# Kernel tuning notes

Measured on AMD Instinct MI355X. Metric: run time of the kernel, lower is better.

## Reference

```python
import jax, jax.numpy as jnp
import numpy as np
from jax import lax

B, T, D_IN, D_PROJ, D_OUT, LORDER = 16, 2048, 1024, 512, 1024, 20


def setup_inputs() -> dict:
    key = jax.random.key(0)
    k1, k2, k3, k4 = jax.random.split(key, 4)
    s = 0.05
    return {
        "input": jax.random.normal(k1, (B, T, D_IN), dtype=jnp.float32),
        "in_cache": jnp.zeros((B, D_PROJ, LORDER - 1), dtype=jnp.float32),
        "W_lin": jax.random.normal(k2, (D_IN, D_PROJ), dtype=jnp.float32) * s,
        "conv_w": jax.random.normal(k3, (D_PROJ, LORDER), dtype=jnp.float32) * s,
        "W_aff": jax.random.normal(k4, (D_PROJ, D_OUT), dtype=jnp.float32) * s,
        "b_aff": jnp.zeros((D_OUT,), dtype=jnp.float32),
    }


def reference(input, in_cache, W_lin, conv_w, W_aff, b_aff):
    L = conv_w.shape[1]
    # 1) linear down-projection (no bias): [B,T,Din] -> [B,T,Dp]
    x = jnp.einsum("btd,dp->btp", input, W_lin)
    # 2) FSMN causal depthwise memory block with streaming cache
    xt = jnp.swapaxes(x, 1, 2)                       # [B,Dp,T]
    cat = jnp.concatenate([in_cache, xt], axis=2)    # [B,Dp,T+L-1]
    out_cache = cat[:, :, -(L - 1):]                 # last L-1 frames for next chunk
    # depthwise conv over time, VALID padding -> output length T
    y = lax.conv_general_dilated(
        cat, conv_w[:, None, :],                      # rhs [Dp,1,L]
        window_strides=(1,), padding="VALID",
        dimension_numbers=("NCH", "OIH", "NCH"),
        feature_group_count=conv_w.shape[0])
    m = jnp.swapaxes(y + xt, 1, 2)                   # residual add, back to [B,T,Dp]
    # 3) affine up-projection + 4) ReLU
    out = jax.nn.relu(jnp.einsum("btp,po->bto", m, W_aff) + b_aff)
    return (out, out_cache)
```

## Files before the change

kernel.cpp:

```cpp
#include <hip/hip_runtime.h>
#include <cstdint>
#include <cstddef>

#define B_  16
#define T_  2048
#define DIN 1024
#define DPJ 512
#define DOUT 1024
#define LORD 20
#define HALO (LORD - 1)
#define M_ROWS (B_ * T_)
#define OUT0_ELEMS ((size_t)M_ROWS * DOUT)
#define CACHE_ELEMS ((size_t)B_ * DPJ * (LORD - 1))

typedef __bf16 bf16_t;
typedef __bf16 bf16x2 __attribute__((ext_vector_type(2)));
typedef __bf16 bf16x4 __attribute__((ext_vector_type(4)));
typedef __bf16 bf16x8 __attribute__((ext_vector_type(8)));
typedef float  f32x4  __attribute__((ext_vector_type(4)));

__device__ __forceinline__ void async_load16(const void* g, void* lds_base) {
    __builtin_amdgcn_global_load_lds(
        (const __attribute__((address_space(1))) unsigned int*)g,
        (__attribute__((address_space(3))) unsigned int*)lds_base,
        16, 0, 0);
}

__device__ __forceinline__ int xcd_swizzle(int hw, int nwg) {
    int cpx = nwg >> 3;
    return (hw & 7) * cpx + (hw >> 3);
}

__global__ __launch_bounds__(256) void prep_weights(
    const float* __restrict__ Wl, const float* __restrict__ Wa,
    bf16_t* __restrict__ WlT, bf16_t* __restrict__ WaT) {
    int idx = blockIdx.x * 256 + threadIdx.x;
    const int n1 = DIN * DPJ;
    if (idx < n1) {
        int n = idx >> 10;
        int k = idx - (n << 10);
        WlT[idx] = (bf16_t)Wl[(size_t)k * DPJ + n];
    } else {
        int j = idx - n1;
        if (j < DPJ * DOUT) {
            int n = j >> 9;
            int k = j - (n << 9);
            WaT[j] = (bf16_t)Wa[(size_t)k * DOUT + n];
        }
    }
}

__global__ __launch_bounds__(512, 4) void gemm1_fused(
    const float* __restrict__ A, const bf16_t* __restrict__ Bt,
    bf16_t* __restrict__ C, const int M, const int N, const int K) {
    __shared__ bf16_t sA[2][128 * 64];
    __shared__ bf16_t sB[2][128 * 64];

    const int tid  = threadIdx.x;
    const int lane = tid & 63;
    const int wave = tid >> 6;

    const int gx   = gridDim.x;
    const int hw   = blockIdx.y * gx + blockIdx.x;
    const int lid  = xcd_swizzle(hw, gx * gridDim.y);
    const int lby  = lid / gx;
    const int lbx  = lid - lby * gx;
    const int col0 = lbx * 128;
    const int row0 = lby * 128;

    const int s4   = tid & 3;
    const int arow = tid >> 2;
    const float* gA = A + (size_t)(row0 + arow) * K + s4 * 8;
    const int o0 = ((s4       ^ (arow & 7)) << 3);
    const int o1 = (((s4 + 4) ^ (arow & 7)) << 3);

    const int lr  = lane >> 3;
    const int jsw = (lane & 7) ^ lr;
    const bf16_t* gB0 = Bt + (size_t)(col0 + wave * 16 + lr) * K + jsw * 8;

    const int wm = (wave >> 2) * 64;
    const int wn = (wave & 3) * 32;
    const int fr = lane & 15;
    const int fk = lane >> 4;

    const f32x4 zero = {0.f, 0.f, 0.f, 0.f};
    f32x4 acc[4][2];
#pragma unroll
    for (int mt = 0; mt < 4; ++mt)
#pragma unroll
        for (int nt = 0; nt < 2; ++nt) acc[mt][nt] = zero;

    f32x4 P[4], Q[4];

    auto load_a = [&](f32x4* r, int kk) {
        r[0] = *(const f32x4*)(gA + kk);
        r[1] = *(const f32x4*)(gA + kk + 4);
        r[2] = *(const f32x4*)(gA + kk + 32);
        r[3] = *(const f32x4*)(gA + kk + 36);
    };
    auto cvt_write = [&](const f32x4* r, bf16_t* dstbuf) {
        bf16x8 v0 = { (bf16_t)r[0][0], (bf16_t)r[0][1], (bf16_t)r[0][2], (bf16_t)r[0][3],
                      (bf16_t)r[1][0], (bf16_t)r[1][1], (bf16_t)r[1][2], (bf16_t)r[1][3] };
        bf16x8 v1 = { (bf16_t)r[2][0], (bf16_t)r[2][1], (bf16_t)r[2][2], (bf16_t)r[2][3],
                      (bf16_t)r[3][0], (bf16_t)r[3][1], (bf16_t)r[3][2], (bf16_t)r[3][3] };
        *(bf16x8*)(dstbuf + arow * 64 + o0) = v0;
        *(bf16x8*)(dstbuf + arow * 64 + o1) = v1;
    };
    auto stage_b = [&](int kk, bf16_t* dstbuf) {
#pragma unroll
        for (int c = 0; c < 2; ++c)
            async_load16(gB0 + (size_t)c * 8 * K + kk, dstbuf + wave * 1024 + c * 512);
    };
    auto compute = [&](const bf16_t* bA, const bf16_t* bB) {
#pragma unroll
        for (int h = 0; h < 2; ++h) {
            bf16x8 af[4], bfr[2];
#pragma unroll
            for (int mt = 0; mt < 4; ++mt) {
                int r = wm + mt * 16 + fr;
                int j = h * 4 + fk;
                af[mt] = *(const bf16x8*)(bA + r * 64 + ((j ^ (r & 7)) << 3));
            }
#pragma unroll
            for (int nt = 0; nt < 2; ++nt) {
                int r = wn + nt * 16 + fr;
                int j = h * 4 + fk;
                bfr[nt] = *(const bf16x8*)(bB + r * 64 + ((j ^ (r & 7)) << 3));
            }
#pragma unroll
            for (int mt = 0; mt < 4; ++mt)
#pragma unroll
                for (int nt = 0; nt < 2; ++nt)
                    acc[mt][nt] = __builtin_amdgcn_mfma_f32_16x16x32_bf16(
                        af[mt], bfr[nt], acc[mt][nt], 0, 0, 0);
        }
    };

    load_a(P, 0);
    stage_b(0, sB[0]);
    cvt_write(P, sA[0]);
    load_a(P, 64);

    for (int k0 = 0; k0 < K; k0 += 128) {
        asm volatile("s_waitcnt vmcnt(4) lgkmcnt(0)" ::: "memory");
        __builtin_amdgcn_sched_barrier(0);
        __builtin_amdgcn_s_barrier();
        __builtin_amdgcn_sched_barrier(0);
        {
            const int kn = k0 + 64;
            stage_b(kn, sB[1]);
            cvt_write(P, sA[1]);
            if (kn + 64 < K) load_a(Q, kn + 64);
        }
        compute(sA[0], sB[0]);

        const int kn2 = k0 + 128;
        if (kn2 >= K) {
            asm volatile("s_waitcnt vmcnt(0) lgkmcnt(0)" ::: "memory");
        } else {
            asm volatile("s_waitcnt vmcnt(4) lgkmcnt(0)" ::: "memory");
        }
        __builtin_amdgcn_sched_barrier(0);
        __builtin_amdgcn_s_barrier();
        __builtin_amdgcn_sched_barrier(0);
        if (kn2 < K) {
            stage_b(kn2, sB[0]);
            cvt_write(Q, sA[0]);
            if (kn2 + 64 < K) load_a(P, kn2 + 64);
        }
        compute(sA[1], sB[1]);
    }

    const int er = row0 + wm + (lane >> 4) * 4;
    const int ec = col0 + wn + (lane & 15);
#pragma unroll
    for (int mt = 0; mt < 4; ++mt)
#pragma unroll
        for (int nt = 0; nt < 2; ++nt)
#pragma unroll
            for (int rr = 0; rr < 4; ++rr)
                C[(size_t)(er + mt * 16 + rr) * N + (ec + nt * 16)] =
                    (bf16_t)acc[mt][nt][rr];
}

__global__ __launch_bounds__(256) void gemm_bt_relu(
    const bf16_t* __restrict__ A, const bf16_t* __restrict__ Bt,
    float* __restrict__ C, const float* __restrict__ bias,
    const int M, const int N, const int K) {
    __shared__ bf16_t sA[2][128 * 64];
    __shared__ bf16_t sB[2][128 * 64];

    const int tid  = threadIdx.x;
    const int lane = tid & 63;
    const int wave = tid >> 6;

    const int gx   = gridDim.x;
    const int hw   = blockIdx.y * gx + blockIdx.x;
    const int lid  = xcd_swizzle(hw, gx * gridDim.y);
    const int lby  = lid / gx;
    const int lbx  = lid - lby * gx;
    const int col0 = lbx * 128;
    const int row0 = lby * 128;

    const int lr   = lane >> 3;
    const int jsw  = (lane & 7) ^ lr;
    const bf16_t* gA0 = A  + (size_t)(row0 + wave * 32 + lr) * K + jsw * 8;
    const bf16_t* gB0 = Bt + (size_t)(col0 + wave * 32 + lr) * K + jsw * 8;

    const int wm = (wave >> 1) * 64;
    const int wn = (wave & 1) * 64;
    const int fr = lane & 15;
    const int fk = lane >> 4;

    const f32x4 zero = {0.f, 0.f, 0.f, 0.f};
    f32x4 acc[4][4];
#pragma unroll
    for (int mt = 0; mt < 4; ++mt)
#pragma unroll
        for (int nt = 0; nt < 4; ++nt) acc[mt][nt] = zero;

    auto stage = [&](int kk, bf16_t* dA, bf16_t* dB) {
#pragma unroll
        for (int c = 0; c < 4; ++c) {
            async_load16(gA0 + (size_t)c * 8 * K + kk, dA + wave * 2048 + c * 512);
            async_load16(gB0 + (size_t)c * 8 * K + kk, dB + wave * 2048 + c * 512);
        }
    };
    auto compute = [&](const bf16_t* bA, const bf16_t* bB) {
#pragma unroll
        for (int h = 0; h < 2; ++h) {
            bf16x8 af[4], bfr[4];
#pragma unroll
            for (int mt = 0; mt < 4; ++mt) {
                int r = wm + mt * 16 + fr;
                int j = h * 4 + fk;
                af[mt] = *(const bf16x8*)(bA + r * 64 + ((j ^ (r & 7)) << 3));
            }
#pragma unroll
            for (int nt = 0; nt < 4; ++nt) {
                int r = wn + nt * 16 + fr;
                int j = h * 4 + fk;
                bfr[nt] = *(const bf16x8*)(bB + r * 64 + ((j ^ (r & 7)) << 3));
            }
#pragma unroll
            for (int mt = 0; mt < 4; ++mt)
#pragma unroll
                for (int nt = 0; nt < 4; ++nt)
                    acc[mt][nt] = __builtin_amdgcn_mfma_f32_16x16x32_bf16(
                        af[mt], bfr[nt], acc[mt][nt], 0, 0, 0);
        }
    };

    stage(0, sA[0], sB[0]);

    for (int k0 = 0; k0 < K; k0 += 128) {
        asm volatile("s_waitcnt vmcnt(0)" ::: "memory");
        __builtin_amdgcn_sched_barrier(0);
        __builtin_amdgcn_s_barrier();
        __builtin_amdgcn_sched_barrier(0);
        stage(k0 + 64, sA[1], sB[1]);
        compute(sA[0], sB[0]);

        asm volatile("s_waitcnt vmcnt(0)" ::: "memory");
        __builtin_amdgcn_sched_barrier(0);
        __builtin_amdgcn_s_barrier();
        __builtin_amdgcn_sched_barrier(0);
        const int kn2 = k0 + 128;
        if (kn2 < K) stage(kn2, sA[0], sB[0]);
        compute(sA[1], sB[1]);
    }

    const int er = row0 + wm + (lane >> 4) * 4;
    const int ec = col0 + wn + (lane & 15);
#pragma unroll
    for (int nt = 0; nt < 4; ++nt) {
        float bb = bias[ec + nt * 16];
#pragma unroll
        for (int mt = 0; mt < 4; ++mt)
#pragma unroll
            for (int rr = 0; rr < 4; ++rr) {
                float v = acc[mt][nt][rr] + bb;
                C[(size_t)(er + mt * 16 + rr) * N + (ec + nt * 16)] =
                    v > 0.f ? v : 0.f;
            }
    }
}

#define TT 64
#define PPT 128
__global__ __launch_bounds__(256) void dwconv_tiled(
    const bf16_t* __restrict__ x, const float* __restrict__ cache,
    const float* __restrict__ cw, bf16_t* __restrict__ m,
    float* __restrict__ oc) {
    __shared__ float sx[(TT + HALO) * PPT];

    const int tid = threadIdx.x;
    const int t0  = blockIdx.x * TT;
    const int b   = blockIdx.y;
    const int p0  = blockIdx.z * PPT;

    for (int c = tid; c < (TT + HALO) * PPT / 8; c += 256) {
        int r    = c >> 4;
        int col  = (c & 15) << 3;
        int trow = t0 - HALO + r;
        float* dst = sx + r * PPT + col;
        if (trow >= 0) {
            bf16x8 v = *(const bf16x8*)(x + ((size_t)(b * T_ + trow)) * DPJ + p0 + col);
#pragma unroll
            for (int i = 0; i < 8; ++i) dst[i] = (float)v[i];
        } else {
#pragma unroll
            for (int i = 0; i < 8; ++i)
                dst[i] = cache[((size_t)b * DPJ + p0 + col + i) * HALO + (trow + HALO)];
        }
    }
    __syncthreads();

    const int pp   = tid & 63;
    const int half = tid >> 6;
    const int tb   = half * 16;
    const float2* sx2 = (const float2*)sx;

    const int pg = p0 + 2 * pp;
    float2 w[LORD];
#pragma unroll
    for (int l = 0; l < LORD; ++l) {
        w[l].x = cw[pg * LORD + l];
        w[l].y = cw[(pg + 1) * LORD + l];
    }

    float2 win[LORD];
#pragma unroll
    for (int i = 0; i < HALO; ++i) win[i] = sx2[(tb + i) * 64 + pp];

#pragma unroll
    for (int tl = 0; tl < 16; ++tl) {
        float2 nv = sx2[(tb + tl + HALO) * 64 + pp];
        win[(tl + HALO) % LORD] = nv;
        float2 s = nv;
#pragma unroll
        for (int l = 0; l < LORD; ++l) {
            float2 v = win[(tl + l) % LORD];
            s.x += w[l].x * v.x;
            s.y += w[l].y * v.y;
        }
        bf16x2 o = { (bf16_t)s.x, (bf16_t)s.y };
        *(bf16x2*)(m + ((size_t)(b * T_ + t0 + tb + tl)) * DPJ + pg) = o;
    }

    if (blockIdx.x == (T_ / TT) - 1) {
        for (int i = tid; i < PPT * HALO; i += 256) {
            int pl = i / HALO;
            int j  = i - pl * HALO;
            oc[((size_t)b * DPJ + p0 + pl) * HALO + j] = sx[(64 + j) * PPT + pl];
        }
    }
}

extern "C" void kernel_launch(void* const* d_in, const int* in_sizes, int n_in,
                              void* d_out, int out_size, void* d_ws, size_t ws_size,
                              hipStream_t stream) {
    const float* input    = (const float*)d_in[0];
    const float* in_cache = (const float*)d_in[1];
    const float* W_lin    = (const float*)d_in[2];
    const float* conv_w   = (const float*)d_in[3];
    const float* W_aff    = (const float*)d_in[4];
    const float* b_aff    = (const float*)d_in[5];
    float* out = (float*)d_out;

    char* ws = (char*)d_ws;
    bf16_t* x_buf = (bf16_t*)(ws);
    bf16_t* m_buf = (bf16_t*)(ws + 33554432);
    bf16_t* WlinT = (bf16_t*)(ws + 67108864);
    bf16_t* WaffT = (bf16_t*)(ws + 67108864 + 1048576);

    prep_weights<<<(DIN * DPJ + DPJ * DOUT + 255) / 256, 256, 0, stream>>>(
        W_lin, W_aff, WlinT, WaffT);

    gemm1_fused<<<dim3(DPJ / 128, M_ROWS / 128), 512, 0, stream>>>(
        input, WlinT, x_buf, M_ROWS, DPJ, DIN);

    dwconv_tiled<<<dim3(T_ / TT, B_, DPJ / PPT), 256, 0, stream>>>(
        x_buf, in_cache, conv_w, m_buf, out + OUT0_ELEMS);

    gemm_bt_relu<<<dim3(DOUT / 128, M_ROWS / 128), 256, 0, stream>>>(
        m_buf, WaffT, out, b_aff, M_ROWS, DOUT, DPJ);
}
```

Baseline: 352.4 us.

## Fuse depthwise FSMN conv into first GEMM with recomputed halo rows

Merges the down-projection GEMM and the depthwise causal conv into one kernel. Each block computes 160 rows (128 plus a 32-row recomputed halo), stages the bf16 result in LDS, and runs the conv from there. This removes the x_buf write/read round trip and one kernel launch. The cost is about 25% redundant GEMM work for the halo rows and a larger LDS footprint (72KB), which may lower occupancy.

```diff
diff --git a/kernel.cpp b/kernel.cpp
--- a/kernel.cpp
+++ b/kernel.cpp
@@ -50,9 +50,209 @@
     }
 }
 
-__global__ __launch_bounds__(512, 4) void gemm1_fused(
+#define XR 160
+#define PADC 136
+__global__ __launch_bounds__(512, 4) void gemm1_conv(
     const float* __restrict__ A, const bf16_t* __restrict__ Bt,
-    bf16_t* __restrict__ C, const int M, const int N, const int K) {
+    const float* __restrict__ cache, const float* __restrict__ cw,
+    bf16_t* __restrict__ m, float* __restrict__ oc) {
+    __shared__ __align__(16) char ldsraw[73728];
+    bf16_t* sA0 = (bf16_t*)(ldsraw);
+    bf16_t* sA1 = (bf16_t*)(ldsraw + 20480);
+    bf16_t* sB0 = (bf16_t*)(ldsraw + 40960);
+    bf16_t* sB1 = (bf16_t*)(ldsraw + 57344);
+    bf16_t* xb  = (bf16_t*)(ldsraw);
+
+    const int tid  = threadIdx.x;
+    const int lane = tid & 63;
+    const int wave = tid >> 6;
+    const int K    = DIN;
+
+    const int gx   = gridDim.x;
+    const int hw   = blockIdx.y * gx + blockIdx.x;
+    const int lid  = xcd_swizzle(hw, gx * gridDim.y);
+    const int lby  = lid / gx;
+    const int lbx  = lid - lby * gx;
+    const int col0 = lbx * 128;
+    const int b    = lby >> 4;
+    const int tloc = (lby & 15) * 128;
+    const float* Ab = A + (size_t)b * T_ * DIN;
+
+    size_t aoff[5];
+    int    doff[5];
+#pragma unroll
+    for (int i = 0; i < 5; ++i) {
+        int u = tid + 512 * i;
+        int r = u >> 4, c16 = u & 15;
+        int t = tloc - 32 + r; if (t < 0) t = 0;
+        aoff[i] = (size_t)t * DIN + c16 * 4;
+        doff[i] = r * 64 + (((c16 >> 1) ^ (r & 7)) << 3) + (c16 & 1) * 4;
+    }
+
+    const int lr  = lane >> 3;
+    const int jsw = (lane & 7) ^ lr;
+    const bf16_t* gB0 = Bt + (size_t)(col0 + wave * 16 + lr) * K + jsw * 8;
+
+    const int wm = (wave >> 2) * 80;
+    const int wn = (wave & 3) * 32;
+    const int fr = lane & 15;
+    const int fk = lane >> 4;
+
+    const f32x4 zero = {0.f, 0.f, 0.f, 0.f};
+    f32x4 acc[5][2];
+#pragma unroll
+    for (int mt = 0; mt < 5; ++mt)
+#pragma unroll
+        for (int nt = 0; nt < 2; ++nt) acc[mt][nt] = zero;
+
+    f32x4 P[5];
+    auto load_a = [&](int kk) {
+#pragma unroll
+        for (int i = 0; i < 5; ++i) P[i] = *(const f32x4*)(Ab + aoff[i] + kk);
+    };
+    auto cvt_write = [&](bf16_t* dst) {
+#pragma unroll
+        for (int i = 0; i < 5; ++i) {
+            bf16x4 v = { (bf16_t)P[i][0], (bf16_t)P[i][1],
+                         (bf16_t)P[i][2], (bf16_t)P[i][3] };
+            *(bf16x4*)(dst + doff[i]) = v;
+        }
+    };
+    auto stage_b = [&](int kk, bf16_t* dstB) {
+#pragma unroll
+        for (int c = 0; c < 2; ++c)
+            async_load16(gB0 + (size_t)c * 8 * K + kk, dstB + wave * 1024 + c * 512);
+    };
+    auto compute = [&](const bf16_t* bA, const bf16_t* bB) {
+#pragma unroll
+        for (int h = 0; h < 2; ++h) {
+            bf16x8 af[5], bfr[2];
+#pragma unroll
+            for (int mt = 0; mt < 5; ++mt) {
+                int r = wm + mt * 16 + fr;
+                int j = h * 4 + fk;
+                af[mt] = *(const bf16x8*)(bA + r * 64 + ((j ^ (r & 7)) << 3));
+            }
+#pragma unroll
+            for (int nt = 0; nt < 2; ++nt) {
+                int r = wn + nt * 16 + fr;
+                int j = h * 4 + fk;
+                bfr[nt] = *(const bf16x8*)(bB + r * 64 + ((j ^ (r & 7)) << 3));
+            }
+#pragma unroll
+            for (int mt = 0; mt < 5; ++mt)
+#pragma unroll
+                for (int nt = 0; nt < 2; ++nt)
+                    acc[mt][nt] = __builtin_amdgcn_mfma_f32_16x16x32_bf16(
+                        af[mt], bfr[nt], acc[mt][nt], 0, 0, 0);
+        }
+    };
+
+    load_a(0);
+    stage_b(0, sB0);
+    cvt_write(sA0);
+    load_a(64);
+
+    for (int k0 = 0; k0 < K; k0 += 128) {
+        asm volatile("s_waitcnt vmcnt(5) lgkmcnt(0)" ::: "memory");
+        __builtin_amdgcn_sched_barrier(0);
+        __builtin_amdgcn_s_barrier();
+        __builtin_amdgcn_sched_barrier(0);
+        stage_b(k0 + 64, sB1);
+        cvt_write(sA1);
+        if (k0 + 128 < K) load_a(k0 + 128);
+        compute(sA0, sB0);
+
+        if (k0 + 128 < K) {
+            asm volatile("s_waitcnt vmcnt(5) lgkmcnt(0)" ::: "memory");
+        } else {
+            asm volatile("s_waitcnt vmcnt(0) lgkmcnt(0)" ::: "memory");
+        }
+        __builtin_amdgcn_sched_barrier(0);
+        __builtin_amdgcn_s_barrier();
+        __builtin_amdgcn_sched_barrier(0);
+        if (k0 + 128 < K) {
+            stage_b(k0 + 128, sB0);
+            cvt_write(sA0);
+            if (k0 + 192 < K) load_a(k0 + 192);
+        }
+        compute(sA1, sB1);
+    }
+
+    __syncthreads();
+    {
+        const int er_l = wm + (lane >> 4) * 4;
+        const int ec_l = wn + (lane & 15);
+#pragma unroll
+        for (int mt = 0; mt < 5; ++mt)
+#pragma unroll
+            for (int nt = 0; nt < 2; ++nt)
+#pragma unroll
+                for (int rr = 0; rr < 4; ++rr)
+                    xb[(er_l + mt * 16 + rr) * PADC + ec_l + nt * 16] =
+                        (bf16_t)acc[mt][nt][rr];
+    }
+    __syncthreads();
+
+    if (tloc == 0) {
+        for (int i2 = tid; i2 < HALO * 128; i2 += 512) {
+            int rr2 = i2 >> 7;
+            int cc  = i2 & 127;
+            xb[(13 + rr2) * PADC + cc] =
+                (bf16_t)cache[((size_t)b * DPJ + col0 + cc) * HALO + rr2];
+        }
+    }
+    __syncthreads();
+
+    {
+        const int pp   = tid & 63;
+        const int tb   = (tid >> 6) * 16;
+        const int pg_l = 2 * pp;
+        const int pg   = col0 + pg_l;
+
+        float2 w[LORD];
+#pragma unroll
+        for (int l = 0; l < LORD; ++l) {
+            w[l].x = cw[pg * LORD + l];
+            w[l].y = cw[(pg + 1) * LORD + l];
+        }
+        auto rdx = [&](int r) -> float2 {
+            bf16x2 v = *(const bf16x2*)(xb + r * PADC + pg_l);
+            float2 f; f.x = (float)v[0]; f.y = (float)v[1]; return f;
+        };
+        float2 win[LORD];
+#pragma unroll
+        for (int i = 0; i < HALO; ++i) win[i] = rdx(tb + 13 + i);
+#pragma unroll
+        for (int tl = 0; tl < 16; ++tl) {
+            float2 nv = rdx(tb + 13 + tl + HALO);
+            win[(tl + HALO) % LORD] = nv;
+            float2 s = nv;
+#pragma unroll
+            for (int l = 0; l < LORD; ++l) {
+                float2 v = win[(tl + l) % LORD];
+                s.x += w[l].x * v.x;
+                s.y += w[l].y * v.y;
+            }
+            bf16x2 o = { (bf16_t)s.x, (bf16_t)s.y };
+            *(bf16x2*)(m + ((size_t)(b * T_ + tloc + tb + tl)) * DPJ + pg) = o;
+        }
+    }
+
+    if (tloc == T_ - 128) {
+        for (int i2 = tid; i2 < 128 * HALO; i2 += 512) {
+            int pl = i2 / HALO;
+            int j  = i2 - pl * HALO;
+            oc[((size_t)b * DPJ + col0 + pl) * HALO + j] =
+                (float)xb[(141 + j) * PADC + pl];
+        }
+    }
+}
+
+__global__ __launch_bounds__(256) void gemm_bt_relu(
+    const bf16_t* __restrict__ A, const bf16_t* __restrict__ Bt,
+    float* __restrict__ C, const float* __restrict__ bias,
+    const int M, const int N, const int K) {
     __shared__ bf16_t sA[2][128 * 64];
     __shared__ bf16_t sB[2][128 * 64];
 
@@ -68,53 +268,34 @@
     const int col0 = lbx * 128;
     const int row0 = lby * 128;
 
-    const int s4   = tid & 3;
-    const int arow = tid >> 2;
-    const float* gA = A + (size_t)(row0 + arow) * K + s4 * 8;
-    const int o0 = ((s4       ^ (arow & 7)) << 3);
-    const int o1 = (((s4 + 4) ^ (arow & 7)) << 3);
-
-    const int lr  = lane >> 3;
-    const int jsw = (lane & 7) ^ lr;
-    const bf16_t* gB0 = Bt + (size_t)(col0 + wave * 16 + lr) * K + jsw * 8;
-
-    const int wm = (wave >> 2) * 64;
-    const int wn = (wave & 3) * 32;
+    const int lr   = lane >> 3;
+    const int jsw  = (lane & 7) ^ lr;
+    const bf16_t* gA0 = A  + (size_t)(row0 + wave * 32 + lr) * K + jsw * 8;
+    const bf16_t* gB0 = Bt + (size_t)(col0 + wave * 32 + lr) * K + jsw * 8;
+
+    const int wm = (wave >> 1) * 64;
+    const int wn = (wave & 1) * 64;
     const int fr = lane & 15;
     const int fk = lane >> 4;
 
     const f32x4 zero = {0.f, 0.f, 0.f, 0.f};
-    f32x4 acc[4][2];
+    f32x4 acc[4][4];
 #pragma unroll
     for (int mt = 0; mt < 4; ++mt)
 #pragma unroll
-        for (int nt = 0; nt < 2; ++nt) acc[mt][nt] = zero;
-
-    f32x4 P[4], Q[4];
-
-    auto load_a = [&](f32x4* r, int kk) {
-        r[0] = *(const f32x4*)(gA + kk);
-        r[1] = *(const f32x4*)(gA + kk + 4);
-        r[2] = *(const f32x4*)(gA + kk + 32);
-        r[3] = *(const f32x4*)(gA + kk + 36);
-    };
-    auto cvt_write = [&](const f32x4* r, bf16_t* dstbuf) {
-        bf16x8 v0 = { (bf16_t)r[0][0], (bf16_t)r[0][1], (bf16_t)r[0][2], (bf16_t)r[0][3],
-                      (bf16_t)r[1][0], (bf16_t)r[1][1], (bf16_t)r[1][2], (bf16_t)r[1][3] };
-        bf16x8 v1 = { (bf16_t)r[2][0], (bf16_t)r[2][1], (bf16_t)r[2][2], (bf16_t)r[2][3],
-                      (bf16_t)r[3][0], (bf16_t)r[3][1], (bf16_t)r[3][2], (bf16_t)r[3][3] };
-        *(bf16x8*)(dstbuf + arow * 64 + o0) = v0;
-        *(bf16x8*)(dstbuf + arow * 64 + o1) = v1;
-    };
-    auto stage_b = [&](int kk, bf16_t* dstbuf) {
-#pragma unroll
-        for (int c = 0; c < 2; ++c)
-            async_load16(gB0 + (size_t)c * 8 * K + kk, dstbuf + wave * 1024 + c * 512);
+        for (int nt = 0; nt < 4; ++nt) acc[mt][nt] = zero;
+
+    auto stage = [&](int kk, bf16_t* dA, bf16_t* dB) {
+#pragma unroll
+        for (int c = 0; c < 4; ++c) {
+            async_load16(gA0 + (size_t)c * 8 * K + kk, dA + wave * 2048 + c * 512);
+            async_load16(gB0 + (size_t)c * 8 * K + kk, dB + wave * 2048 + c * 512);
+        }
     };
     auto compute = [&](const bf16_t* bA, const bf16_t* bB) {
 #pragma unroll
         for (int h = 0; h < 2; ++h) {
-            bf16x8 af[4], bfr[2];
+            bf16x8 af[4], bfr[4];
 #pragma unroll
             for (int mt = 0; mt < 4; ++mt) {
                 int r = wm + mt * 16 + fr;
@@ -122,121 +303,6 @@
                 af[mt] = *(const bf16x8*)(bA + r * 64 + ((j ^ (r & 7)) << 3));
             }
 #pragma unroll
-            for (int nt = 0; nt < 2; ++nt) {
-                int r = wn + nt * 16 + fr;
-                int j = h * 4 + fk;
-                bfr[nt] = *(const bf16x8*)(bB + r * 64 + ((j ^ (r & 7)) << 3));
-            }
-#pragma unroll
-            for (int mt = 0; mt < 4; ++mt)
-#pragma unroll
-                for (int nt = 0; nt < 2; ++nt)
-                    acc[mt][nt] = __builtin_amdgcn_mfma_f32_16x16x32_bf16(
-                        af[mt], bfr[nt], acc[mt][nt], 0, 0, 0);
-        }
-    };
-
-    load_a(P, 0);
-    stage_b(0, sB[0]);
-    cvt_write(P, sA[0]);
-    load_a(P, 64);
-
-    for (int k0 = 0; k0 < K; k0 += 128) {
-        asm volatile("s_waitcnt vmcnt(4) lgkmcnt(0)" ::: "memory");
-        __builtin_amdgcn_sched_barrier(0);
-        __builtin_amdgcn_s_barrier();
-        __builtin_amdgcn_sched_barrier(0);
-        {
-            const int kn = k0 + 64;
-            stage_b(kn, sB[1]);
-            cvt_write(P, sA[1]);
-            if (kn + 64 < K) load_a(Q, kn + 64);
-        }
-        compute(sA[0], sB[0]);
-
-        const int kn2 = k0 + 128;
-        if (kn2 >= K) {
-            asm volatile("s_waitcnt vmcnt(0) lgkmcnt(0)" ::: "memory");
-        } else {
-            asm volatile("s_waitcnt vmcnt(4) lgkmcnt(0)" ::: "memory");
-        }
-        __builtin_amdgcn_sched_barrier(0);
-        __builtin_amdgcn_s_barrier();
-        __builtin_amdgcn_sched_barrier(0);
-        if (kn2 < K) {
-            stage_b(kn2, sB[0]);
-            cvt_write(Q, sA[0]);
-            if (kn2 + 64 < K) load_a(P, kn2 + 64);
-        }
-        compute(sA[1], sB[1]);
-    }
-
-    const int er = row0 + wm + (lane >> 4) * 4;
-    const int ec = col0 + wn + (lane & 15);
-#pragma unroll
-    for (int mt = 0; mt < 4; ++mt)
-#pragma unroll
-        for (int nt = 0; nt < 2; ++nt)
-#pragma unroll
-            for (int rr = 0; rr < 4; ++rr)
-                C[(size_t)(er + mt * 16 + rr) * N + (ec + nt * 16)] =
-                    (bf16_t)acc[mt][nt][rr];
-}
-
-__global__ __launch_bounds__(256) void gemm_bt_relu(
-    const bf16_t* __restrict__ A, const bf16_t* __restrict__ Bt,
-    float* __restrict__ C, const float* __restrict__ bias,
-    const int M, const int N, const int K) {
-    __shared__ bf16_t sA[2][128 * 64];
-    __shared__ bf16_t sB[2][128 * 64];
-
-    const int tid  = threadIdx.x;
-    const int lane = tid & 63;
-    const int wave = tid >> 6;
-
-    const int gx   = gridDim.x;
-    const int hw   = blockIdx.y * gx + blockIdx.x;
-    const int lid  = xcd_swizzle(hw, gx * gridDim.y);
-    const int lby  = lid / gx;
-    const int lbx  = lid - lby * gx;
-    const int col0 = lbx * 128;
-    const int row0 = lby * 128;
-
-    const int lr   = lane >> 3;
-    const int jsw  = (lane & 7) ^ lr;
-    const bf16_t* gA0 = A  + (size_t)(row0 + wave * 32 + lr) * K + jsw * 8;
-    const bf16_t* gB0 = Bt + (size_t)(col0 + wave * 32 + lr) * K + jsw * 8;
-
-    const int wm = (wave >> 1) * 64;
-    const int wn = (wave & 1) * 64;
-    const int fr = lane & 15;
-    const int fk = lane >> 4;
-
-    const f32x4 zero = {0.f, 0.f, 0.f, 0.f};
-    f32x4 acc[4][4];
-#pragma unroll
-    for (int mt = 0; mt < 4; ++mt)
-#pragma unroll
-        for (int nt = 0; nt < 4; ++nt) acc[mt][nt] = zero;
-
-    auto stage = [&](int kk, bf16_t* dA, bf16_t* dB) {
-#pragma unroll
-        for (int c = 0; c < 4; ++c) {
-            async_load16(gA0 + (size_t)c * 8 * K + kk, dA + wave * 2048 + c * 512);
-            async_load16(gB0 + (size_t)c * 8 * K + kk, dB + wave * 2048 + c * 512);
-        }
-    };
-    auto compute = [&](const bf16_t* bA, const bf16_t* bB) {
-#pragma unroll
-        for (int h = 0; h < 2; ++h) {
-            bf16x8 af[4], bfr[4];
-#pragma unroll
-            for (int mt = 0; mt < 4; ++mt) {
-                int r = wm + mt * 16 + fr;
-                int j = h * 4 + fk;
-                af[mt] = *(const bf16x8*)(bA + r * 64 + ((j ^ (r & 7)) << 3));
-            }
-#pragma unroll
             for (int nt = 0; nt < 4; ++nt) {
                 int r = wn + nt * 16 + fr;
                 int j = h * 4 + fk;
@@ -283,77 +349,6 @@
                 C[(size_t)(er + mt * 16 + rr) * N + (ec + nt * 16)] =
                     v > 0.f ? v : 0.f;
             }
-    }
-}
-
-#define TT 64
-#define PPT 128
-__global__ __launch_bounds__(256) void dwconv_tiled(
-    const bf16_t* __restrict__ x, const float* __restrict__ cache,
-    const float* __restrict__ cw, bf16_t* __restrict__ m,
-    float* __restrict__ oc) {
-    __shared__ float sx[(TT + HALO) * PPT];
-
-    const int tid = threadIdx.x;
-    const int t0  = blockIdx.x * TT;
-    const int b   = blockIdx.y;
-    const int p0  = blockIdx.z * PPT;
-
-    for (int c = tid; c < (TT + HALO) * PPT / 8; c += 256) {
-        int r    = c >> 4;
-        int col  = (c & 15) << 3;
-        int trow = t0 - HALO + r;
-        float* dst = sx + r * PPT + col;
-        if (trow >= 0) {
-            bf16x8 v = *(const bf16x8*)(x + ((size_t)(b * T_ + trow)) * DPJ + p0 + col);
-#pragma unroll
-            for (int i = 0; i < 8; ++i) dst[i] = (float)v[i];
-        } else {
-#pragma unroll
-            for (int i = 0; i < 8; ++i)
-                dst[i] = cache[((size_t)b * DPJ + p0 + col + i) * HALO + (trow + HALO)];
-        }
-    }
-    __syncthreads();
-
-    const int pp   = tid & 63;
-    const int half = tid >> 6;
-    const int tb   = half * 16;
-    const float2* sx2 = (const float2*)sx;
-
-    const int pg = p0 + 2 * pp;
-    float2 w[LORD];
-#pragma unroll
-    for (int l = 0; l < LORD; ++l) {
-        w[l].x = cw[pg * LORD + l];
-        w[l].y = cw[(pg + 1) * LORD + l];
-    }
-
-    float2 win[LORD];
-#pragma unroll
-    for (int i = 0; i < HALO; ++i) win[i] = sx2[(tb + i) * 64 + pp];
-
-#pragma unroll
-    for (int tl = 0; tl < 16; ++tl) {
-        float2 nv = sx2[(tb + tl + HALO) * 64 + pp];
-        win[(tl + HALO) % LORD] = nv;
-        float2 s = nv;
-#pragma unroll
-        for (int l = 0; l < LORD; ++l) {
-            float2 v = win[(tl + l) % LORD];
-            s.x += w[l].x * v.x;
-            s.y += w[l].y * v.y;
-        }
-        bf16x2 o = { (bf16_t)s.x, (bf16_t)s.y };
-        *(bf16x2*)(m + ((size_t)(b * T_ + t0 + tb + tl)) * DPJ + pg) = o;
-    }
-
-    if (blockIdx.x == (T_ / TT) - 1) {
-        for (int i = tid; i < PPT * HALO; i += 256) {
-            int pl = i / HALO;
-            int j  = i - pl * HALO;
-            oc[((size_t)b * DPJ + p0 + pl) * HALO + j] = sx[(64 + j) * PPT + pl];
-        }
     }
 }
 
@@ -369,7 +364,6 @@
     float* out = (float*)d_out;
 
     char* ws = (char*)d_ws;
-    bf16_t* x_buf = (bf16_t*)(ws);
     bf16_t* m_buf = (bf16_t*)(ws + 33554432);
     bf16_t* WlinT = (bf16_t*)(ws + 67108864);
     bf16_t* WaffT = (bf16_t*)(ws + 67108864 + 1048576);
@@ -377,11 +371,8 @@
     prep_weights<<<(DIN * DPJ + DPJ * DOUT + 255) / 256, 256, 0, stream>>>(
         W_lin, W_aff, WlinT, WaffT);
 
-    gemm1_fused<<<dim3(DPJ / 128, M_ROWS / 128), 512, 0, stream>>>(
-        input, WlinT, x_buf, M_ROWS, DPJ, DIN);
-
-    dwconv_tiled<<<dim3(T_ / TT, B_, DPJ / PPT), 256, 0, stream>>>(
-        x_buf, in_cache, conv_w, m_buf, out + OUT0_ELEMS);
+    gemm1_conv<<<dim3(DPJ / 128, M_ROWS / 128), 512, 0, stream>>>(
+        input, WlinT, in_cache, conv_w, m_buf, out + OUT0_ELEMS);
 
     gemm_bt_relu<<<dim3(DOUT / 128, M_ROWS / 128), 256, 0, stream>>>(
         m_buf, WaffT, out, b_aff, M_ROWS, DOUT, DPJ);
```

Result: faster. 332.7 us (-5.6%).
